# Kernel tuning notes

Measured on AMD Instinct MI355X. Metric: run time of the kernel, lower is better.

The kernel has to match this reference:

```python
import jax, jax.numpy as jnp
import numpy as np

N = 100000      # nodes
E = 1_600_000   # edges (avg degree 16)
DIMS = [(64, 64), (64, 64), (64, 40)]  # gnn_layers [64,64,64,40]


def setup_inputs() -> dict:
    key = jax.random.key(0)
    ks = jax.random.split(key, 2 + 3 * len(DIMS))
    inp = {
        "x": jax.random.normal(ks[0], (N, DIMS[0][0]), jnp.float32),
        "edge_index": jax.random.randint(ks[1], (2, E), 0, N),
    }
    k = 2
    for i, (din, dout) in enumerate(DIMS):
        s = 1.0 / np.sqrt(din)
        inp[f"Wl{i}"] = jax.random.uniform(ks[k], (din, dout), jnp.float32, -s, s); k += 1
        inp[f"bl{i}"] = jax.random.uniform(ks[k], (dout,), jnp.float32, -s, s); k += 1
        inp[f"Wr{i}"] = jax.random.uniform(ks[k], (din, dout), jnp.float32, -s, s); k += 1
    return inp


def _sage_conv(x, src, dst, Wl, bl, Wr):
    # PyG SAGEConv (mean aggr): out = lin_l(mean_{j in N(i)} x_j) + lin_r(x_i)
    deg = jax.ops.segment_sum(jnp.ones((src.shape[0],), x.dtype), dst, num_segments=N)
    agg = jax.ops.segment_sum(x[src], dst, num_segments=N)  # [N, din] scatter-add
    agg = agg / jnp.clip(deg, 1.0)[:, None]                  # mean; isolated nodes -> 0
    return agg @ Wl + bl + x @ Wr


def reference(x, edge_index, Wl0, bl0, Wr0, Wl1, bl1, Wr1, Wl2, bl2, Wr2):
    src, dst = edge_index[0], edge_index[1]
    h = x
    params = [(Wl0, bl0, Wr0), (Wl1, bl1, Wr1), (Wl2, bl2, Wr2)]
    for i, (Wl, bl, Wr) in enumerate(params):
        h = _sage_conv(h, src, dst, Wl, bl, Wr)
        if i != len(params) - 1:
            h = jax.nn.relu(h)
            # F.dropout with training=False is identity (eval mode)
    return jax.nn.log_softmax(h, axis=1)
```

## Files before the change

### kernel.cpp

```cpp
#include <hip/hip_runtime.h>
#include <math.h>

#define ACT_RELU 0
#define ACT_LSM  1
#define BSH 8
#define MAXNB 512
#define MPAD 80

typedef __attribute__((ext_vector_type(8))) short bf16x8;
typedef __attribute__((ext_vector_type(4))) float f32x4;

__device__ __forceinline__ unsigned f2bf(float f) {
  unsigned u = __float_as_uint(f);
  u += 0x7fffu + ((u >> 16) & 1u);
  return u >> 16;
}
__device__ __forceinline__ float bflo(unsigned u) { return __uint_as_float(u << 16); }
__device__ __forceinline__ float bfhi(unsigned u) { return __uint_as_float(u & 0xffff0000u); }

__global__ void k_zero(int* __restrict__ p, int n) {
  int i = blockIdx.x * 256 + threadIdx.x;
  if (i < n) p[i] = 0;
}

__global__ void k_histB(const int* __restrict__ dst, int* __restrict__ bucket_cnt,
                        int E, int NB) {
  __shared__ int cntL[MAXNB];
  int t = threadIdx.x;
  for (int b = t; b < NB; b += 256) cntL[b] = 0;
  __syncthreads();
  int e0 = blockIdx.x * 4096;
  int e1 = min(e0 + 4096, E);
  for (int i = e0 + t; i < e1; i += 256) atomicAdd(&cntL[dst[i] >> BSH], 1);
  __syncthreads();
  for (int b = t; b < NB; b += 256)
    if (cntL[b]) atomicAdd(&bucket_cnt[b], cntL[b]);
}

__global__ void k_bscan(const int* __restrict__ bucket_cnt, int* __restrict__ bucket_base,
                        int* __restrict__ bucket_cursor, int NB) {
  __shared__ int sm[MAXNB];
  int t = threadIdx.x;
  sm[t] = (t < NB) ? bucket_cnt[t] : 0;
  __syncthreads();
  for (int off = 1; off < MAXNB; off <<= 1) {
    int x = (t >= off) ? sm[t - off] : 0;
    __syncthreads();
    sm[t] += x;
    __syncthreads();
  }
  int ex = (t == 0) ? 0 : sm[t - 1];
  if (t <= NB) bucket_base[t] = ex;
  if (t < NB) bucket_cursor[t] = ex;
}

__global__ void k_partition(const int* __restrict__ src, const int* __restrict__ dst,
                            int* __restrict__ bucket_cursor, int2* __restrict__ tmp,
                            int E, int NB) {
  __shared__ int cntL[MAXNB];
  __shared__ int baseL[MAXNB];
  int t = threadIdx.x;
  for (int b = t; b < NB; b += 256) cntL[b] = 0;
  __syncthreads();
  int e0 = blockIdx.x * 4096;
  int e1 = min(e0 + 4096, E);
  for (int i = e0 + t; i < e1; i += 256) atomicAdd(&cntL[dst[i] >> BSH], 1);
  __syncthreads();
  for (int b = t; b < NB; b += 256) {
    int c = cntL[b];
    baseL[b] = c ? atomicAdd(&bucket_cursor[b], c) : 0;
    cntL[b] = 0;
  }
  __syncthreads();
  for (int i = e0 + t; i < e1; i += 256) {
    int s = src[i], d = dst[i];
    int b = d >> BSH;
    int r = atomicAdd(&cntL[b], 1);
    tmp[baseL[b] + r] = make_int2(s, d);
  }
}

__global__ void __launch_bounds__(256) k_bmake(const int2* __restrict__ tmp,
                                               const int* __restrict__ bucket_base,
                                               int* __restrict__ row_ptr,
                                               int* __restrict__ edge_src,
                                               int N, int E, int NB) {
  __shared__ int cntL[256];
  __shared__ int scanL[256];
  int b = blockIdx.x;
  int t = threadIdx.x;
  int e0 = bucket_base[b], e1 = bucket_base[b + 1];
  cntL[t] = 0;
  __syncthreads();
  for (int i = e0 + t; i < e1; i += 256) atomicAdd(&cntL[tmp[i].y & 255], 1);
  __syncthreads();
  int v = cntL[t];
  scanL[t] = v;
  __syncthreads();
  for (int off = 1; off < 256; off <<= 1) {
    int x = (t >= off) ? scanL[t - off] : 0;
    __syncthreads();
    scanL[t] += x;
    __syncthreads();
  }
  int exc = scanL[t] - v;
  int node = (b << BSH) + t;
  if (node < N) row_ptr[node] = e0 + exc;
  if (b == NB - 1 && t == 0) row_ptr[N] = E;
  __syncthreads();
  cntL[t] = e0 + exc;
  __syncthreads();
  for (int i = e0 + t; i < e1; i += 256) {
    int2 e = tmp[i];
    int p = atomicAdd(&cntL[e.y & 255], 1);
    edge_src[p] = e.x;
  }
}

__global__ void k_hist(const int* __restrict__ dst, int* __restrict__ cnt, int E) {
  int i = blockIdx.x * blockDim.x + threadIdx.x;
  if (i < E) atomicAdd(&cnt[dst[i]], 1);
}

__global__ void k_scan_part(const int* __restrict__ cnt, int* __restrict__ bsum, int M) {
  __shared__ int sm[256];
  int t = threadIdx.x;
  int base = blockIdx.x * 2048 + t * 8;
  int s = 0;
#pragma unroll
  for (int j = 0; j < 8; ++j) { int i = base + j; if (i < M) s += cnt[i]; }
  sm[t] = s;
  __syncthreads();
  for (int off = 128; off > 0; off >>= 1) {
    if (t < off) sm[t] += sm[t + off];
    __syncthreads();
  }
  if (t == 0) bsum[blockIdx.x] = sm[0];
}

__global__ void k_scan_mid(const int* __restrict__ bsum, int* __restrict__ boff, int nb) {
  int l = threadIdx.x;
  int v = (l < nb) ? bsum[l] : 0;
  int inc = v;
  for (int off = 1; off < 64; off <<= 1) {
    int u = __shfl_up(inc, off);
    if (l >= off) inc += u;
  }
  if (l < nb) boff[l] = inc - v;
}

__global__ void k_scan_final(const int* __restrict__ cnt, const int* __restrict__ boff,
                             int* __restrict__ row_ptr, int* __restrict__ cursor, int M) {
  __shared__ int sm[256];
  int t = threadIdx.x;
  int base = blockIdx.x * 2048 + t * 8;
  int v[8];
  int s = 0;
#pragma unroll
  for (int j = 0; j < 8; ++j) { int i = base + j; v[j] = (i < M) ? cnt[i] : 0; s += v[j]; }
  sm[t] = s;
  __syncthreads();
  for (int off = 1; off < 256; off <<= 1) {
    int x = (t >= off) ? sm[t - off] : 0;
    __syncthreads();
    sm[t] += x;
    __syncthreads();
  }
  int run = boff[blockIdx.x] + sm[t] - s;
#pragma unroll
  for (int j = 0; j < 8; ++j) {
    int i = base + j;
    if (i < M) { row_ptr[i] = run; cursor[i] = run; }
    run += v[j];
  }
}

__global__ void k_fill(const int* __restrict__ src, const int* __restrict__ dst,
                       int* __restrict__ cursor, int* __restrict__ edge_src, int E) {
  int i = blockIdx.x * blockDim.x + threadIdx.x;
  if (i < E) {
    int d = dst[i];
    int p = atomicAdd(&cursor[d], 1);
    edge_src[p] = src[i];
  }
}

__global__ void __launch_bounds__(256) k_cast(const float* __restrict__ x,
                                              unsigned short* __restrict__ xb, int n) {
  int i = blockIdx.x * 256 + threadIdx.x;
  if (i * 8 < n) {
    const float4* p = (const float4*)(x + (size_t)i * 8);
    float4 a = p[0], b = p[1];
    uint4 w;
    w.x = f2bf(a.x) | (f2bf(a.y) << 16);
    w.y = f2bf(a.z) | (f2bf(a.w) << 16);
    w.z = f2bf(b.x) | (f2bf(b.y) << 16);
    w.w = f2bf(b.z) | (f2bf(b.w) << 16);
    *(uint4*)(xb + (size_t)i * 8) = w;
  }
}

template <int DOUT>
__global__ void k_prepw(const float* __restrict__ Wl, const float* __restrict__ Wr,
                        unsigned short* __restrict__ Wb) {
  constexpr int NT = (DOUT + 15) / 16;
  constexpr int PADN = NT * 16;
  int fi = blockIdx.x * 256 + threadIdx.x;
  if (fi < 128 * PADN) {
    int k7 = fi & 7;
    int kb = (fi >> 3) & 3;
    int c16 = (fi >> 5) & 15;
    int rest = fi >> 9;
    int nt = rest % NT;
    int kb5 = rest / NT;
    int k = kb5 * 32 + kb * 8 + k7;
    int nn = nt * 16 + c16;
    float v = 0.f;
    if (nn < DOUT) v = (k < 64) ? Wl[k * DOUT + nn] : Wr[(k - 64) * DOUT + nn];
    Wb[fi] = (unsigned short)f2bf(v);
  }
}

template <int DOUT, int ACT>
__global__ void __launch_bounds__(256) k_layer(const unsigned short* __restrict__ h,
                                               const int* __restrict__ row_ptr,
                                               const int* __restrict__ edge_src,
                                               const unsigned short* __restrict__ Wb,
                                               const float* __restrict__ bias,
                                               void* __restrict__ outv, int n) {
  constexpr int NT = (DOUT + 15) / 16;
  __shared__ unsigned short meanL[4][16 * MPAD];
  int t = threadIdx.x;
  int w = t >> 6, lane = t & 63;
  int r0 = (blockIdx.x * 4 + w) * 16;
  int g = lane & 7;

  for (int half = 0; half < 2; ++half) {
    int node = half * 8 + (lane >> 3);
    int i = r0 + node;
    float a[8];
#pragma unroll
    for (int c = 0; c < 8; ++c) a[c] = 0.f;
    float scale = 0.f;
    if (i < n) {
      int rp0 = row_ptr[i], rp1 = row_ptr[i + 1];
      int deg = rp1 - rp0;
      scale = (deg > 0) ? (1.0f / (float)deg) : 0.f;
      for (int base = 0; base < deg; base += 8) {
        int idx = rp0 + base + g;
        int sv = (idx < rp1) ? edge_src[idx] : 0;
        int cnt = min(8, deg - base);
        uint4 v0, v1, v2, v3, v4, v5, v6, v7;
#pragma unroll
        for (int e = 0; e < 8; ++e) {
          int s = __shfl(sv, (lane & ~7) | e);
          const uint4* p = (const uint4*)(h + (size_t)s * 64) + g;
          if (e == 0 && e < cnt) v0 = *p;
          if (e == 1 && e < cnt) v1 = *p;
          if (e == 2 && e < cnt) v2 = *p;
          if (e == 3 && e < cnt) v3 = *p;
          if (e == 4 && e < cnt) v4 = *p;
          if (e == 5 && e < cnt) v5 = *p;
          if (e == 6 && e < cnt) v6 = *p;
          if (e == 7 && e < cnt) v7 = *p;
        }
#define ACCUM(vv, ee)                                                   \
        if ((ee) < cnt) {                                               \
          a[0] += bflo(vv.x); a[1] += bfhi(vv.x);                       \
          a[2] += bflo(vv.y); a[3] += bfhi(vv.y);                       \
          a[4] += bflo(vv.z); a[5] += bfhi(vv.z);                       \
          a[6] += bflo(vv.w); a[7] += bfhi(vv.w);                       \
        }
        ACCUM(v0, 0) ACCUM(v1, 1) ACCUM(v2, 2) ACCUM(v3, 3)
        ACCUM(v4, 4) ACCUM(v5, 5) ACCUM(v6, 6) ACCUM(v7, 7)
#undef ACCUM
      }
    }
    uint4 wv;
    wv.x = f2bf(a[0] * scale) | (f2bf(a[1] * scale) << 16);
    wv.y = f2bf(a[2] * scale) | (f2bf(a[3] * scale) << 16);
    wv.z = f2bf(a[4] * scale) | (f2bf(a[5] * scale) << 16);
    wv.w = f2bf(a[6] * scale) | (f2bf(a[7] * scale) << 16);
    *(uint4*)&meanL[w][node * MPAD + g * 8] = wv;
  }
  __threadfence_block();

  int c = lane & 15;
  int kb = lane >> 4;
  bf16x8 af[4];
  af[0] = *(const bf16x8*)&meanL[w][c * MPAD + kb * 8];
  af[1] = *(const bf16x8*)&meanL[w][c * MPAD + 32 + kb * 8];
  int row = r0 + c;
  if (row >= n) row = n - 1;
  size_t rb = (size_t)row * 64 + kb * 8;
  af[2] = *(const bf16x8*)(h + rb);
  af[3] = *(const bf16x8*)(h + rb + 32);

  f32x4 acc[NT];
#pragma unroll
  for (int nt = 0; nt < NT; ++nt) acc[nt] = (f32x4){0.f, 0.f, 0.f, 0.f};
#pragma unroll
  for (int s = 0; s < 4; ++s) {
    bf16x8 bft[NT];
#pragma unroll
    for (int nt = 0; nt < NT; ++nt)
      bft[nt] = *(const bf16x8*)&Wb[(((s * NT + nt) * 16 + c) * 4 + kb) * 8];
#pragma unroll
    for (int nt = 0; nt < NT; ++nt)
      acc[nt] = __builtin_amdgcn_mfma_f32_16x16x32_bf16(af[s], bft[nt], acc[nt], 0, 0, 0);
  }

  int rbase = r0 + kb * 4;
  if (ACT == ACT_RELU) {
    unsigned short* out = (unsigned short*)outv;
#pragma unroll
    for (int nt = 0; nt < NT; ++nt) {
      float bval = bias[nt * 16 + c];
#pragma unroll
      for (int r = 0; r < 4; ++r) {
        int R = rbase + r;
        if (R < n) {
          float v = fmaxf(acc[nt][r] + bval, 0.f);
          out[(size_t)R * DOUT + nt * 16 + c] = (unsigned short)f2bf(v);
        }
      }
    }
  } else {
    float* out = (float*)outv;
    float bv[NT];
#pragma unroll
    for (int nt = 0; nt < NT; ++nt) bv[nt] = ((nt * 16 + c) < DOUT) ? bias[nt * 16 + c] : 0.f;
#pragma unroll
    for (int r = 0; r < 4; ++r) {
      int R = rbase + r;
      float v[NT];
      float m = -INFINITY;
#pragma unroll
      for (int nt = 0; nt < NT; ++nt) {
        bool valid = (nt * 16 + c) < DOUT;
        v[nt] = valid ? (acc[nt][r] + bv[nt]) : -INFINITY;
        m = fmaxf(m, v[nt]);
      }
#pragma unroll
      for (int off = 1; off < 16; off <<= 1) m = fmaxf(m, __shfl_xor(m, off));
      float es = 0.f;
#pragma unroll
      for (int nt = 0; nt < NT; ++nt)
        if ((nt * 16 + c) < DOUT) es += expf(v[nt] - m);
#pragma unroll
      for (int off = 1; off < 16; off <<= 1) es += __shfl_xor(es, off);
      float lse = logf(es);
      if (R < n) {
#pragma unroll
        for (int nt = 0; nt < NT; ++nt)
          if ((nt * 16 + c) < DOUT) out[(size_t)R * DOUT + nt * 16 + c] = v[nt] - m - lse;
      }
    }
  }
}

extern "C" void kernel_launch(void* const* d_in, const int* in_sizes, int n_in,
                              void* d_out, int out_size, void* d_ws, size_t ws_size,
                              hipStream_t stream) {
  const float* x   = (const float*)d_in[0];
  const int*   ei  = (const int*)d_in[1];
  const float* Wl0 = (const float*)d_in[2];
  const float* bl0 = (const float*)d_in[3];
  const float* Wr0 = (const float*)d_in[4];
  const float* Wl1 = (const float*)d_in[5];
  const float* bl1 = (const float*)d_in[6];
  const float* Wr1 = (const float*)d_in[7];
  const float* Wl2 = (const float*)d_in[8];
  const float* bl2 = (const float*)d_in[9];
  const float* Wr2 = (const float*)d_in[10];
  float* out = (float*)d_out;

  int N = in_sizes[0] / 64;
  int E = in_sizes[1] / 2;
  int M = N + 1;
  int NB = (N + 255) >> BSH;
  const int* src = ei;
  const int* dst = ei + E;

  char* p = (char*)d_ws;
  auto alloc = [&](size_t bytes) {
    char* r = p;
    p += (bytes + 255) & ~(size_t)255;
    return r;
  };
  int* cnt      = (int*)alloc((size_t)M * 4);
  int* row_ptr  = (int*)alloc((size_t)M * 4);
  int* cursor   = (int*)alloc((size_t)M * 4);
  int* bsum     = (int*)alloc(256 * 4);
  int* boff     = (int*)alloc(256 * 4);
  int* bk_cnt   = (int*)alloc((MAXNB + 1) * 4);
  int* bk_base  = (int*)alloc((MAXNB + 1) * 4);
  int* bk_cur   = (int*)alloc((MAXNB + 1) * 4);
  int* edge_src = (int*)alloc((size_t)E * 4);
  size_t szR1 = (size_t)E * 8 > (size_t)N * 128 ? (size_t)E * 8 : (size_t)N * 128;
  char* R1              = alloc(szR1);
  unsigned short* hbA   = (unsigned short*)alloc((size_t)N * 128);
  unsigned short* Wb0   = (unsigned short*)alloc(128 * 64 * 2);
  unsigned short* Wb1   = (unsigned short*)alloc(128 * 64 * 2);
  unsigned short* Wb2   = (unsigned short*)alloc(128 * 48 * 2);
  if ((size_t)(p - (char*)d_ws) > ws_size) return;

  bool bucketed = (NB <= MAXNB);
  int eb4 = (E + 4095) / 4096;

  k_prepw<64><<<(128 * 64 + 255) / 256, 256, 0, stream>>>(Wl0, Wr0, Wb0);
  k_prepw<64><<<(128 * 64 + 255) / 256, 256, 0, stream>>>(Wl1, Wr1, Wb1);
  k_prepw<40><<<(128 * 48 + 255) / 256, 256, 0, stream>>>(Wl2, Wr2, Wb2);

  if (bucketed) {
    k_zero<<<(MAXNB + 256) / 256, 256, 0, stream>>>(bk_cnt, MAXNB + 1);
    k_histB<<<eb4, 256, 0, stream>>>(dst, bk_cnt, E, NB);
    k_bscan<<<1, MAXNB, 0, stream>>>(bk_cnt, bk_base, bk_cur, NB);
    k_partition<<<eb4, 256, 0, stream>>>(src, dst, bk_cur, (int2*)R1, E, NB);
    k_bmake<<<NB, 256, 0, stream>>>((const int2*)R1, bk_base, row_ptr, edge_src, N, E, NB);
  } else {
    k_zero<<<(M + 255) / 256, 256, 0, stream>>>(cnt, M);
    k_hist<<<(E + 255) / 256, 256, 0, stream>>>(dst, cnt, E);
    int nb = (M + 2047) / 2048;
    k_scan_part<<<nb, 256, 0, stream>>>(cnt, bsum, M);
    k_scan_mid<<<1, 64, 0, stream>>>(bsum, boff, nb);
    k_scan_final<<<nb, 256, 0, stream>>>(cnt, boff, row_ptr, cursor, M);
    k_fill<<<(E + 255) / 256, 256, 0, stream>>>(src, dst, cursor, edge_src, E);
  }

  unsigned short* xb  = (unsigned short*)R1;
  unsigned short* hbB = (unsigned short*)R1;

  int cb = (N * 64 / 8 + 255) / 256;
  int gb = (N + 63) / 64;

  k_cast<<<cb, 256, 0, stream>>>(x, xb, N * 64);
  k_layer<64, ACT_RELU><<<gb, 256, 0, stream>>>(xb, row_ptr, edge_src, Wb0, bl0, hbA, N);
  k_layer<64, ACT_RELU><<<gb, 256, 0, stream>>>(hbA, row_ptr, edge_src, Wb1, bl1, hbB, N);
  k_layer<40, ACT_LSM><<<gb, 256, 0, stream>>>(hbB, row_ptr, edge_src, Wb2, bl2, out, N);
}
```

Before: 196.2 us.

## Pack bucket edges into 32-bit words, halve rows per wave, merge weight prep

The partition temp buffer now stores each edge as one 32-bit word (source shifted left by 8, OR'd with the low 8 bits of the destination) instead of an int2. This halves the scratch traffic between the partition and bucket-build kernels, and a guard limits this path to N below 2^24. Each wave in the layer kernel now aggregates 8 nodes instead of 16, doubling the grid so more waves hide gather latency. Half of each MFMA tile is then wasted on duplicated rows, whose stores are masked off. The three weight-prep launches are merged into one kernel to cut launch overhead.

```diff
diff --git a/kernel.cpp b/kernel.cpp
--- a/kernel.cpp
+++ b/kernel.cpp
@@ -55,7 +55,7 @@
 }
 
 __global__ void k_partition(const int* __restrict__ src, const int* __restrict__ dst,
-                            int* __restrict__ bucket_cursor, int2* __restrict__ tmp,
+                            int* __restrict__ bucket_cursor, unsigned* __restrict__ tmp,
                             int E, int NB) {
   __shared__ int cntL[MAXNB];
   __shared__ int baseL[MAXNB];
@@ -76,11 +76,11 @@
     int s = src[i], d = dst[i];
     int b = d >> BSH;
     int r = atomicAdd(&cntL[b], 1);
-    tmp[baseL[b] + r] = make_int2(s, d);
-  }
-}
-
-__global__ void __launch_bounds__(256) k_bmake(const int2* __restrict__ tmp,
+    tmp[baseL[b] + r] = ((unsigned)s << 8) | (unsigned)(d & 255);
+  }
+}
+
+__global__ void __launch_bounds__(256) k_bmake(const unsigned* __restrict__ tmp,
                                                const int* __restrict__ bucket_base,
                                                int* __restrict__ row_ptr,
                                                int* __restrict__ edge_src,
@@ -92,7 +92,7 @@
   int e0 = bucket_base[b], e1 = bucket_base[b + 1];
   cntL[t] = 0;
   __syncthreads();
-  for (int i = e0 + t; i < e1; i += 256) atomicAdd(&cntL[tmp[i].y & 255], 1);
+  for (int i = e0 + t; i < e1; i += 256) atomicAdd(&cntL[tmp[i] & 255], 1);
   __syncthreads();
   int v = cntL[t];
   scanL[t] = v;
@@ -111,9 +111,9 @@
   cntL[t] = e0 + exc;
   __syncthreads();
   for (int i = e0 + t; i < e1; i += 256) {
-    int2 e = tmp[i];
-    int p = atomicAdd(&cntL[e.y & 255], 1);
-    edge_src[p] = e.x;
+    unsigned e = tmp[i];
+    int p = atomicAdd(&cntL[e & 255], 1);
+    edge_src[p] = (int)(e >> 8);
   }
 }
 
@@ -200,25 +200,31 @@
   }
 }
 
-template <int DOUT>
-__global__ void k_prepw(const float* __restrict__ Wl, const float* __restrict__ Wr,
-                        unsigned short* __restrict__ Wb) {
-  constexpr int NT = (DOUT + 15) / 16;
-  constexpr int PADN = NT * 16;
-  int fi = blockIdx.x * 256 + threadIdx.x;
-  if (fi < 128 * PADN) {
-    int k7 = fi & 7;
-    int kb = (fi >> 3) & 3;
-    int c16 = (fi >> 5) & 15;
-    int rest = fi >> 9;
-    int nt = rest % NT;
-    int kb5 = rest / NT;
-    int k = kb5 * 32 + kb * 8 + k7;
-    int nn = nt * 16 + c16;
-    float v = 0.f;
-    if (nn < DOUT) v = (k < 64) ? Wl[k * DOUT + nn] : Wr[(k - 64) * DOUT + nn];
-    Wb[fi] = (unsigned short)f2bf(v);
-  }
+__device__ __forceinline__ void prepw_one(const float* Wl, const float* Wr,
+                                          unsigned short* Wb, int fi, int DOUT, int NT) {
+  int k7 = fi & 7;
+  int kb = (fi >> 3) & 3;
+  int c16 = (fi >> 5) & 15;
+  int rest = fi >> 9;
+  int nt = rest % NT;
+  int kb5 = rest / NT;
+  int k = kb5 * 32 + kb * 8 + k7;
+  int nn = nt * 16 + c16;
+  float v = 0.f;
+  if (nn < DOUT) v = (k < 64) ? Wl[k * DOUT + nn] : Wr[(k - 64) * DOUT + nn];
+  Wb[fi] = (unsigned short)f2bf(v);
+}
+
+__global__ void k_prepw3(const float* __restrict__ Wl0, const float* __restrict__ Wr0,
+                         unsigned short* __restrict__ Wb0,
+                         const float* __restrict__ Wl1, const float* __restrict__ Wr1,
+                         unsigned short* __restrict__ Wb1,
+                         const float* __restrict__ Wl2, const float* __restrict__ Wr2,
+                         unsigned short* __restrict__ Wb2) {
+  int i = blockIdx.x * 256 + threadIdx.x;
+  if (i < 8192) prepw_one(Wl0, Wr0, Wb0, i, 64, 4);
+  else if (i < 16384) prepw_one(Wl1, Wr1, Wb1, i - 8192, 64, 4);
+  else if (i < 22528) prepw_one(Wl2, Wr2, Wb2, i - 16384, 40, 3);
 }
 
 template <int DOUT, int ACT>
@@ -229,14 +235,14 @@
                                                const float* __restrict__ bias,
                                                void* __restrict__ outv, int n) {
   constexpr int NT = (DOUT + 15) / 16;
-  __shared__ unsigned short meanL[4][16 * MPAD];
+  __shared__ unsigned short meanL[4][8 * MPAD];
   int t = threadIdx.x;
   int w = t >> 6, lane = t & 63;
-  int r0 = (blockIdx.x * 4 + w) * 16;
+  int r0 = (blockIdx.x * 4 + w) * 8;
   int g = lane & 7;
-
-  for (int half = 0; half < 2; ++half) {
-    int node = half * 8 + (lane >> 3);
+  int node = lane >> 3;
+
+  {
     int i = r0 + node;
     float a[8];
 #pragma unroll
@@ -286,11 +292,12 @@
   __threadfence_block();
 
   int c = lane & 15;
+  int c8 = c & 7;
   int kb = lane >> 4;
   bf16x8 af[4];
-  af[0] = *(const bf16x8*)&meanL[w][c * MPAD + kb * 8];
-  af[1] = *(const bf16x8*)&meanL[w][c * MPAD + 32 + kb * 8];
-  int row = r0 + c;
+  af[0] = *(const bf16x8*)&meanL[w][c8 * MPAD + kb * 8];
+  af[1] = *(const bf16x8*)&meanL[w][c8 * MPAD + 32 + kb * 8];
+  int row = r0 + c8;
   if (row >= n) row = n - 1;
   size_t rb = (size_t)row * 64 + kb * 8;
   af[2] = *(const bf16x8*)(h + rb);
@@ -311,6 +318,7 @@
   }
 
   int rbase = r0 + kb * 4;
+  bool rowv = (kb < 2);
   if (ACT == ACT_RELU) {
     unsigned short* out = (unsigned short*)outv;
 #pragma unroll
@@ -319,7 +327,7 @@
 #pragma unroll
       for (int r = 0; r < 4; ++r) {
         int R = rbase + r;
-        if (R < n) {
+        if (rowv && R < n) {
           float v = fmaxf(acc[nt][r] + bval, 0.f);
           out[(size_t)R * DOUT + nt * 16 + c] = (unsigned short)f2bf(v);
         }
@@ -350,7 +358,7 @@
 #pragma unroll
       for (int off = 1; off < 16; off <<= 1) es += __shfl_xor(es, off);
       float lse = logf(es);
-      if (R < n) {
+      if (rowv && R < n) {
 #pragma unroll
         for (int nt = 0; nt < NT; ++nt)
           if ((nt * 16 + c) < DOUT) out[(size_t)R * DOUT + nt * 16 + c] = v[nt] - m - lse;
@@ -397,7 +405,7 @@
   int* bk_base  = (int*)alloc((MAXNB + 1) * 4);
   int* bk_cur   = (int*)alloc((MAXNB + 1) * 4);
   int* edge_src = (int*)alloc((size_t)E * 4);
-  size_t szR1 = (size_t)E * 8 > (size_t)N * 128 ? (size_t)E * 8 : (size_t)N * 128;
+  size_t szR1 = (size_t)E * 4 > (size_t)N * 128 ? (size_t)E * 4 : (size_t)N * 128;
   char* R1              = alloc(szR1);
   unsigned short* hbA   = (unsigned short*)alloc((size_t)N * 128);
   unsigned short* Wb0   = (unsigned short*)alloc(128 * 64 * 2);
@@ -405,19 +413,18 @@
   unsigned short* Wb2   = (unsigned short*)alloc(128 * 48 * 2);
   if ((size_t)(p - (char*)d_ws) > ws_size) return;
 
-  bool bucketed = (NB <= MAXNB);
+  bool bucketed = (NB <= MAXNB) && (N < (1 << 24));
   int eb4 = (E + 4095) / 4096;
 
-  k_prepw<64><<<(128 * 64 + 255) / 256, 256, 0, stream>>>(Wl0, Wr0, Wb0);
-  k_prepw<64><<<(128 * 64 + 255) / 256, 256, 0, stream>>>(Wl1, Wr1, Wb1);
-  k_prepw<40><<<(128 * 48 + 255) / 256, 256, 0, stream>>>(Wl2, Wr2, Wb2);
+  k_prepw3<<<(22528 + 255) / 256, 256, 0, stream>>>(Wl0, Wr0, Wb0, Wl1, Wr1, Wb1,
+                                                    Wl2, Wr2, Wb2);
 
   if (bucketed) {
     k_zero<<<(MAXNB + 256) / 256, 256, 0, stream>>>(bk_cnt, MAXNB + 1);
     k_histB<<<eb4, 256, 0, stream>>>(dst, bk_cnt, E, NB);
     k_bscan<<<1, MAXNB, 0, stream>>>(bk_cnt, bk_base, bk_cur, NB);
-    k_partition<<<eb4, 256, 0, stream>>>(src, dst, bk_cur, (int2*)R1, E, NB);
-    k_bmake<<<NB, 256, 0, stream>>>((const int2*)R1, bk_base, row_ptr, edge_src, N, E, NB);
+    k_partition<<<eb4, 256, 0, stream>>>(src, dst, bk_cur, (unsigned*)R1, E, NB);
+    k_bmake<<<NB, 256, 0, stream>>>((const unsigned*)R1, bk_base, row_ptr, edge_src, N, E, NB);
   } else {
     k_zero<<<(M + 255) / 256, 256, 0, stream>>>(cnt, M);
     k_hist<<<(E + 255) / 256, 256, 0, stream>>>(dst, cnt, E);
@@ -432,7 +439,7 @@
   unsigned short* hbB = (unsigned short*)R1;
 
   int cb = (N * 64 / 8 + 255) / 256;
-  int gb = (N + 63) / 64;
+  int gb = (N + 31) / 32;
 
   k_cast<<<cb, 256, 0, stream>>>(x, xb, N * 64);
   k_layer<64, ACT_RELU><<<gb, 256, 0, stream>>>(xb, row_ptr, edge_src, Wb0, bl0, hbA, N);
```

Result: slower. 211.8 us (+7.9%).
